# Performance work log

Hardware: AMD Instinct MI355X
Metric: run time of the kernel (lower is better)

Reference implementation:

```python
import jax, jax.numpy as jnp
import numpy as np

EPS = 1e-6
H, HD = 16, 64

def layernorm(x):
    m = jnp.mean(x, -1, keepdims=True)
    v = jnp.mean((x - m) ** 2, -1, keepdims=True)
    return (x - m) * jax.lax.rsqrt(v + EPS)

def rmsnorm(x, w):
    return x * jax.lax.rsqrt(jnp.mean(x * x, -1, keepdims=True) + EPS) * w

def apply_rope(x, rope_emb):
    # x: [B,S,H,D], rope_emb: [S,1,1,D] with cos||sin halves
    half = rope_emb.shape[-1] // 2
    cos = jnp.transpose(rope_emb[..., :half], (1, 0, 2, 3))  # [1,S,1,half]
    sin = jnp.transpose(rope_emb[..., half:], (1, 0, 2, 3))
    x1, x2 = x[..., :half], x[..., half:]
    rotated = jnp.concatenate([-x2, x1], -1)
    return x * jnp.concatenate([cos, cos], -1) + rotated * jnp.concatenate([sin, sin], -1)

def attention(xq, ctx, wq, wk, wv, wo, qn, kn, rope_emb):
    B, S, _ = xq.shape
    M = ctx.shape[1]
    q = (xq @ wq.T).reshape(B, S, H, HD)
    k = (ctx @ wk.T).reshape(B, M, H, HD)
    v = (ctx @ wv.T).reshape(B, M, H, HD)
    q = rmsnorm(q, qn)
    k = rmsnorm(k, kn)
    if rope_emb is not None:  # self-attn only
        q = apply_rope(q, rope_emb)
        k = apply_rope(k, rope_emb)
    # explicit bf16 cast before SDPA, as in torch_attention_op
    qb, kb, vb = (t.astype(jnp.bfloat16) for t in (q, k, v))
    scale = 1.0 / np.sqrt(HD).astype(np.float32)
    scores = jnp.einsum('bqhd,bkhd->bhqk', qb, kb) * scale
    probs = jax.nn.softmax(scores.astype(jnp.float32), -1).astype(jnp.bfloat16)
    out = jnp.einsum('bhqk,bkhd->bqhd', probs, vb)  # [B,S,H,HD]
    out = out.reshape(B, S, H * HD).astype(jnp.float32)
    return out @ wo.T

def modulation(emb, w):
    y = jax.nn.silu(emb) @ w.T  # [B, 3D]
    shift, scale, gate = jnp.split(y, 3, axis=-1)
    return shift[:, None], scale[:, None], gate[:, None]  # [B,1,D]

def setup_inputs() -> dict:
    key = jax.random.key(0)
    B, S, D, M, DF = 1, 4096, 1024, 512, 4096
    ks = jax.random.split(key, 20)
    std_d = 1.0 / np.sqrt(D)
    inp = {
        'x': jax.random.normal(ks[0], (B, S, D), jnp.float32),
        'emb': jax.random.normal(ks[1], (B, D), jnp.float32),
        'crossattn_emb': jax.random.normal(ks[2], (B, M, D), jnp.float32),
        'sa_wq': jax.random.normal(ks[3], (D, D), jnp.float32) * std_d,
        'sa_wk': jax.random.normal(ks[4], (D, D), jnp.float32) * std_d,
        'sa_wv': jax.random.normal(ks[5], (D, D), jnp.float32) * std_d,
        'sa_wo': jax.random.normal(ks[6], (D, D), jnp.float32) * std_d,
        'sa_qn': jnp.ones((HD,), jnp.float32),
        'sa_kn': jnp.ones((HD,), jnp.float32),
        'ca_wq': jax.random.normal(ks[7], (D, D), jnp.float32) * std_d,
        'ca_wk': jax.random.normal(ks[8], (D, D), jnp.float32) * std_d,
        'ca_wv': jax.random.normal(ks[9], (D, D), jnp.float32) * std_d,
        'ca_wo': jax.random.normal(ks[10], (D, D), jnp.float32) * std_d,
        'ca_qn': jnp.ones((HD,), jnp.float32),
        'ca_kn': jnp.ones((HD,), jnp.float32),
        'mlp_w1': jax.random.normal(ks[11], (DF, D), jnp.float32) * std_d,
        'mlp_w2': jax.random.normal(ks[12], (D, DF), jnp.float32) * (1.0 / np.sqrt(DF)),
        'mod_sa_w': jax.random.normal(ks[13], (3 * D, D), jnp.float32) * 0.02,
        'mod_ca_w': jax.random.normal(ks[14], (3 * D, D), jnp.float32) * 0.02,
        'mod_mlp_w': jax.random.normal(ks[15], (3 * D, D), jnp.float32) * 0.02,
    }
    # RoPE table [S,1,1,HD]: first half cos, second half sin
    pos = jnp.arange(S, dtype=jnp.float32)
    inv_freq = 1.0 / (10000.0 ** (jnp.arange(0, HD // 2, dtype=jnp.float32) / (HD // 2)))
    ang = pos[:, None] * inv_freq[None, :]  # [S, HD/2]
    inp['rope_emb'] = jnp.concatenate([jnp.cos(ang), jnp.sin(ang)], -1)[:, None, None, :]
    return inp

def reference(x, emb, crossattn_emb, rope_emb, sa_wq, sa_wk, sa_wv, sa_wo, sa_qn, sa_kn,
              ca_wq, ca_wk, ca_wv, ca_wo, ca_qn, ca_kn, mlp_w1, mlp_w2,
              mod_sa_w, mod_ca_w, mod_mlp_w):
    # self-attn with adaln modulation
    sh, sc, g = modulation(emb, mod_sa_w)
    h = layernorm(x) * (1.0 + sc) + sh
    x = x + g * attention(h, h, sa_wq, sa_wk, sa_wv, sa_wo, sa_qn, sa_kn, rope_emb)
    # cross-attn
    sh, sc, g = modulation(emb, mod_ca_w)
    h = layernorm(x) * (1.0 + sc) + sh
    x = x + g * attention(h, crossattn_emb, ca_wq, ca_wk, ca_wv, ca_wo, ca_qn, ca_kn, None)
    # mlp
    sh, sc, g = modulation(emb, mod_mlp_w)
    h = layernorm(x) * (1.0 + sc) + sh
    x = x + g * (jax.nn.gelu(h @ mlp_w1.T, approximate=False) @ mlp_w2.T)
    return x
```

## Files before the change

### kernel.cpp

```cpp
#include <hip/hip_runtime.h>
#include <hip/hip_bf16.h>

typedef __attribute__((ext_vector_type(8))) __bf16 bf16x8;
typedef __attribute__((ext_vector_type(4))) float f32x4;
typedef __attribute__((ext_vector_type(4))) unsigned short us4;

__device__ __forceinline__ unsigned short f2bf(float f){
  union { float f; unsigned int u; } a; a.f = f;
  unsigned int r = 0x7fffu + ((a.u >> 16) & 1u);
  return (unsigned short)((a.u + r) >> 16);
}

__device__ __forceinline__ unsigned int cvt_pk_bf16(float lo, float hi){
  unsigned int d;
  asm("v_cvt_pk_bf16_f32 %0, %1, %2" : "=v"(d) : "v"(lo), "v"(hi));
  return d;
}

__device__ __forceinline__ float exp2_hw(float x){
  float d;
  asm("v_exp_f32 %0, %1" : "=v"(d) : "v"(x));
  return d;
}

__device__ __forceinline__ void gload_lds16(const unsigned short* g, void* l){
  __builtin_amdgcn_global_load_lds(
      (const __attribute__((address_space(1))) void*)g,
      (__attribute__((address_space(3))) void*)l, 16, 0, 0);
}

struct CastJobs {
  const float* src[11];
  unsigned short* dst[11];
  int blkStart[12];
};

__global__ __launch_bounds__(256) void cast_all_kernel(CastJobs jobs){
  int bid = blockIdx.x;
  int j = 0;
  #pragma unroll
  for (int i = 0; i < 11; i++) j += (bid >= jobs.blkStart[i + 1]) ? 1 : 0;
  int i4 = (bid - jobs.blkStart[j]) * 256 + threadIdx.x;
  float4 v = ((const float4*)jobs.src[j])[i4];
  us4 o; o.x = f2bf(v.x); o.y = f2bf(v.y); o.z = f2bf(v.z); o.w = f2bf(v.w);
  ((us4*)jobs.dst[j])[i4] = o;
}

__global__ __launch_bounds__(256) void modulation_kernel(const float* __restrict__ emb,
    const float* __restrict__ w0, const float* __restrict__ w1, const float* __restrict__ w2,
    float* __restrict__ out){
  int gw = blockIdx.x * 4 + (threadIdx.x >> 6);
  int lane = threadIdx.x & 63;
  int mat = gw / 3072, row = gw % 3072;
  const float* w = (mat == 0) ? w0 : (mat == 1 ? w1 : w2);
  float acc = 0.f;
  for (int i = lane; i < 1024; i += 64){
    float e = emb[i];
    float s = e / (1.f + expf(-e));
    acc += s * w[row * 1024 + i];
  }
  #pragma unroll
  for (int m = 32; m >= 1; m >>= 1) acc += __shfl_xor(acc, m, 64);
  if (lane == 0) out[mat * 3072 + row] = acc;
}

__global__ __launch_bounds__(256) void ln_mod_kernel(const float* __restrict__ x,
    const float* __restrict__ mod, unsigned short* __restrict__ h){
  int row = blockIdx.x, t = threadIdx.x;
  const float* xr = x + (size_t)row * 1024;
  float4 v = ((const float4*)xr)[t];
  float s = v.x + v.y + v.z + v.w;
  #pragma unroll
  for (int m = 32; m >= 1; m >>= 1) s += __shfl_xor(s, m, 64);
  __shared__ float red[4], red2[4];
  int wid = t >> 6, lane = t & 63;
  if (lane == 0) red[wid] = s;
  __syncthreads();
  float mean = (red[0] + red[1] + red[2] + red[3]) * (1.f / 1024.f);
  float dx = v.x - mean, dy = v.y - mean, dz = v.z - mean, dw = v.w - mean;
  float s2 = dx*dx + dy*dy + dz*dz + dw*dw;
  #pragma unroll
  for (int m = 32; m >= 1; m >>= 1) s2 += __shfl_xor(s2, m, 64);
  if (lane == 0) red2[wid] = s2;
  __syncthreads();
  float var = (red2[0] + red2[1] + red2[2] + red2[3]) * (1.f / 1024.f);
  float rs = rsqrtf(var + 1e-6f);
  int c = t * 4;
  us4 o;
  o.x = f2bf(dx * rs * (1.f + mod[1024 + c    ]) + mod[c    ]);
  o.y = f2bf(dy * rs * (1.f + mod[1024 + c + 1]) + mod[c + 1]);
  o.z = f2bf(dz * rs * (1.f + mod[1024 + c + 2]) + mod[c + 2]);
  o.w = f2bf(dw * rs * (1.f + mod[1024 + c + 3]) + mod[c + 3]);
  ((us4*)(h + (size_t)row * 1024))[t] = o;
}

template<int ROPE>
__global__ __launch_bounds__(256) void qk_post2_kernel(
    const float* __restrict__ qin, const float* __restrict__ qnw,
    const float* __restrict__ kin, const float* __restrict__ knw,
    const float* __restrict__ rope,
    unsigned short* __restrict__ qout, unsigned short* __restrict__ kout,
    int Sq, int Sk, int qblocks){
  int bid = blockIdx.x;
  const float* in; const float* nw; unsigned short* out; int S;
  if (bid < qblocks){ in = qin; nw = qnw; out = qout; S = Sq; }
  else { in = kin; nw = knw; out = kout; S = Sk; bid -= qblocks; }
  int gw = bid * 4 + (threadIdx.x >> 6);
  int lane = threadIdx.x & 63;
  int s = gw >> 4, h = gw & 15;
  float v = in[(size_t)s * 1024 + h * 64 + lane];
  float ss = v * v;
  #pragma unroll
  for (int m = 32; m >= 1; m >>= 1) ss += __shfl_xor(ss, m, 64);
  float val = v * rsqrtf(ss * (1.f / 64.f) + 1e-6f) * nw[lane];
  if (ROPE){
    float partner = __shfl_xor(val, 32, 64);
    float cs = rope[s * 64 + (lane & 31)];
    float sn = rope[s * 64 + 32 + (lane & 31)];
    val = (lane < 32) ? (val * cs - partner * sn) : (val * cs + partner * sn);
  }
  out[((size_t)h * S + s) * 64 + lane] = f2bf(val);
}

__global__ __launch_bounds__(256) void vt_kernel(const float* __restrict__ Vf,
    unsigned short* __restrict__ Vt, int S){
  int stile = blockIdx.x, h = blockIdx.y;
  __shared__ unsigned short tile[64 * 66];
  int t = threadIdx.x;
  #pragma unroll
  for (int i = 0; i < 16; i++){
    int e = i * 256 + t;
    int srow = e >> 6, d = e & 63;
    tile[d * 66 + srow] = f2bf(Vf[(size_t)(stile * 64 + srow) * 1024 + h * 64 + d]);
  }
  __syncthreads();
  #pragma unroll
  for (int i = 0; i < 16; i++){
    int e = i * 256 + t;
    int d = e >> 6, scol = e & 63;
    Vt[((size_t)h * 64 + d) * S + stile * 64 + scol] = tile[d * 66 + scol];
  }
}

template<int EPI>
__global__ __launch_bounds__(256) void gemm_bt_kernel(
    const unsigned short* __restrict__ A, const unsigned short* __restrict__ W,
    int M, int N, int K,
    float* __restrict__ outF, unsigned short* __restrict__ outB,
    const float* __restrict__ resid, const float* __restrict__ gate){
  __shared__ short As[128 * 64];
  __shared__ short Bs[128 * 64];
  const int t = threadIdx.x, wid = t >> 6, lane = t & 63;
  const int r = lane & 15, g = lane >> 4;
  const int brow = blockIdx.y * 128, bcol = blockIdx.x * 128;
  const int wr = wid >> 1, wc = wid & 1;
  f32x4 acc[4][4] = {};
  const int nkt = K >> 6;
  for (int kt = 0; kt < nkt; ++kt){
    const int k0 = kt << 6;
    #pragma unroll
    for (int i = 0; i < 4; i++){
      int chunk = wid * 4 + i;
      int rowi = chunk * 8 + (lane >> 3);
      int lce = ((lane & 7) * 8) ^ ((rowi & 7) << 3);
      gload_lds16(A + (size_t)(brow + rowi) * K + k0 + lce, (void*)(As + chunk * 512));
      gload_lds16(W + (size_t)(bcol + rowi) * K + k0 + lce, (void*)(Bs + chunk * 512));
    }
    __syncthreads();
    #pragma unroll
    for (int kk = 0; kk < 2; kk++){
      bf16x8 af[4], bfr[4];
      #pragma unroll
      for (int m = 0; m < 4; m++){
        int ar = wr * 64 + m * 16 + r;
        af[m] = *(const bf16x8*)(As + ar * 64 + ((kk * 32 + g * 8) ^ ((ar & 7) << 3)));
      }
      #pragma unroll
      for (int n = 0; n < 4; n++){
        int br = wc * 64 + n * 16 + r;
        bfr[n] = *(const bf16x8*)(Bs + br * 64 + ((kk * 32 + g * 8) ^ ((br & 7) << 3)));
      }
      #pragma unroll
      for (int m = 0; m < 4; m++)
        #pragma unroll
        for (int n = 0; n < 4; n++)
          acc[m][n] = __builtin_amdgcn_mfma_f32_16x16x32_bf16(af[m], bfr[n], acc[m][n], 0, 0, 0);
    }
    __syncthreads();
  }
  #pragma unroll
  for (int m = 0; m < 4; m++){
    #pragma unroll
    for (int n = 0; n < 4; n++){
      int col = bcol + wc * 64 + n * 16 + r;
      #pragma unroll
      for (int j = 0; j < 4; j++){
        int rowj = brow + wr * 64 + m * 16 + g * 4 + j;
        float v = acc[m][n][j];
        if (EPI == 0){
          outF[(size_t)rowj * N + col] = v;
        } else if (EPI == 2){
          float gl = 0.5f * v * (1.f + erff(v * 0.70710678118654752f));
          outB[(size_t)rowj * N + col] = f2bf(gl);
        } else if (EPI == 4){
          outF[(size_t)(col >> 10) * 4194304 + (size_t)rowj * 1024 + (col & 1023)] = v;
        } else {
          outF[(size_t)rowj * N + col] = resid[(size_t)rowj * N + col] + gate[col] * v;
        }
      }
    }
  }
}

template<int EPI>
__global__ __launch_bounds__(256) void gemm_bt64_kernel(
    const unsigned short* __restrict__ A, const unsigned short* __restrict__ W,
    int M, int N, int K,
    float* __restrict__ outF, unsigned short* __restrict__ outB,
    const float* __restrict__ resid, const float* __restrict__ gate){
  __shared__ short As[64 * 64];
  __shared__ short Bs[128 * 64];
  const int t = threadIdx.x, wid = t >> 6, lane = t & 63;
  const int r = lane & 15, g = lane >> 4;
  const int brow = blockIdx.y * 64, bcol = blockIdx.x * 128;
  f32x4 acc[4][2] = {};
  const int nkt = K >> 6;
  const int sr = lane >> 3;
  const int lce = ((lane & 7) * 8) ^ ((sr & 7) << 3);
  for (int kt = 0; kt < nkt; ++kt){
    const int k0 = kt << 6;
    #pragma unroll
    for (int i = 0; i < 2; i++){
      int chunk = wid * 2 + i;
      gload_lds16(A + (size_t)(brow + chunk * 8 + sr) * K + k0 + lce, (void*)(As + chunk * 512));
    }
    #pragma unroll
    for (int i = 0; i < 4; i++){
      int chunk = wid * 4 + i;
      gload_lds16(W + (size_t)(bcol + chunk * 8 + sr) * K + k0 + lce, (void*)(Bs + chunk * 512));
    }
    __syncthreads();
    #pragma unroll
    for (int kk = 0; kk < 2; kk++){
      bf16x8 af[4], bfr[2];
      #pragma unroll
      for (int m = 0; m < 4; m++){
        int ar = m * 16 + r;
        af[m] = *(const bf16x8*)(As + ar * 64 + ((kk * 32 + g * 8) ^ ((ar & 7) << 3)));
      }
      #pragma unroll
      for (int n = 0; n < 2; n++){
        int br = wid * 32 + n * 16 + r;
        bfr[n] = *(const bf16x8*)(Bs + br * 64 + ((kk * 32 + g * 8) ^ ((br & 7) << 3)));
      }
      #pragma unroll
      for (int m = 0; m < 4; m++)
        #pragma unroll
        for (int n = 0; n < 2; n++)
          acc[m][n] = __builtin_amdgcn_mfma_f32_16x16x32_bf16(af[m], bfr[n], acc[m][n], 0, 0, 0);
    }
    __syncthreads();
  }
  #pragma unroll
  for (int m = 0; m < 4; m++){
    #pragma unroll
    for (int n = 0; n < 2; n++){
      int col = bcol + wid * 32 + n * 16 + r;
      #pragma unroll
      for (int j = 0; j < 4; j++){
        int rowj = brow + m * 16 + g * 4 + j;
        float v = acc[m][n][j];
        if (EPI == 0){
          outF[(size_t)rowj * N + col] = v;
        } else if (EPI == 4){
          outF[(size_t)(col >> 10) * 4194304 + (size_t)rowj * 1024 + (col & 1023)] = v;
        } else {
          outF[(size_t)rowj * N + col] = resid[(size_t)rowj * N + col] + gate[col] * v;
        }
      }
    }
  }
}

__global__ __launch_bounds__(256) void gemm_bt64_sk_kernel(
    const unsigned short* __restrict__ A, const unsigned short* __restrict__ W,
    int M, int N, int K, float* __restrict__ outP){
  __shared__ short As[64 * 64];
  __shared__ short Bs[128 * 64];
  const int t = threadIdx.x, wid = t >> 6, lane = t & 63;
  const int r = lane & 15, g = lane >> 4;
  const int brow = blockIdx.y * 64, bcol = blockIdx.x * 128;
  const int zk = blockIdx.z;
  const int koff = zk * (K >> 1);
  float* out = outP + (size_t)zk * 4194304;
  f32x4 acc[4][2] = {};
  const int nkt = K >> 7;
  const int sr = lane >> 3;
  const int lce = ((lane & 7) * 8) ^ ((sr & 7) << 3);
  for (int kt = 0; kt < nkt; ++kt){
    const int k0 = koff + (kt << 6);
    #pragma unroll
    for (int i = 0; i < 2; i++){
      int chunk = wid * 2 + i;
      gload_lds16(A + (size_t)(brow + chunk * 8 + sr) * K + k0 + lce, (void*)(As + chunk * 512));
    }
    #pragma unroll
    for (int i = 0; i < 4; i++){
      int chunk = wid * 4 + i;
      gload_lds16(W + (size_t)(bcol + chunk * 8 + sr) * K + k0 + lce, (void*)(Bs + chunk * 512));
    }
    __syncthreads();
    #pragma unroll
    for (int kk = 0; kk < 2; kk++){
      bf16x8 af[4], bfr[2];
      #pragma unroll
      for (int m = 0; m < 4; m++){
        int ar = m * 16 + r;
        af[m] = *(const bf16x8*)(As + ar * 64 + ((kk * 32 + g * 8) ^ ((ar & 7) << 3)));
      }
      #pragma unroll
      for (int n = 0; n < 2; n++){
        int br = wid * 32 + n * 16 + r;
        bfr[n] = *(const bf16x8*)(Bs + br * 64 + ((kk * 32 + g * 8) ^ ((br & 7) << 3)));
      }
      #pragma unroll
      for (int m = 0; m < 4; m++)
        #pragma unroll
        for (int n = 0; n < 2; n++)
          acc[m][n] = __builtin_amdgcn_mfma_f32_16x16x32_bf16(af[m], bfr[n], acc[m][n], 0, 0, 0);
    }
    __syncthreads();
  }
  #pragma unroll
  for (int m = 0; m < 4; m++){
    #pragma unroll
    for (int n = 0; n < 2; n++){
      int col = bcol + wid * 32 + n * 16 + r;
      #pragma unroll
      for (int j = 0; j < 4; j++){
        int rowj = brow + m * 16 + g * 4 + j;
        out[(size_t)rowj * N + col] = acc[m][n][j];
      }
    }
  }
}

__global__ __launch_bounds__(256) void reduce_gg_kernel(const float* __restrict__ p0,
    const float* __restrict__ p1, const float* __restrict__ gate, float* __restrict__ xio){
  int i4 = blockIdx.x * 256 + threadIdx.x;
  float4 a = ((const float4*)p0)[i4];
  float4 b = ((const float4*)p1)[i4];
  float4 rr = ((const float4*)xio)[i4];
  int col = (i4 * 4) & 1023;
  float4 gv = *(const float4*)&gate[col];
  float4 o;
  o.x = rr.x + gv.x * (a.x + b.x);
  o.y = rr.y + gv.y * (a.y + b.y);
  o.z = rr.z + gv.z * (a.z + b.z);
  o.w = rr.w + gv.w * (a.w + b.w);
  ((float4*)xio)[i4] = o;
}

__global__ __launch_bounds__(256) void attn_kernel(
    const unsigned short* __restrict__ Qb, const unsigned short* __restrict__ Kb,
    const unsigned short* __restrict__ Vtg, unsigned short* __restrict__ Out,
    int Sq, int Skv){
  __shared__ short Ks[3][4096];
  __shared__ short Vs[3][4096];
  __shared__ unsigned short Ps[4][2048];
  const int t = threadIdx.x, wid = t >> 6, lane = t & 63;
  const int r = lane & 15, g = lane >> 4;
  const int bid = blockIdx.x;
  const int slot = bid >> 3;
  const int h = (bid & 7) * 2 + (slot >> 5);
  const int qblk = slot & 31;
  const int qbase = qblk * 128 + wid * 32;
  const float SC = 0.18033688f;
  const float MS = 12.0f;

  const int srow0 = wid * 16 + (lane >> 3);
  const int scol  = ((lane & 7) * 8) ^ (((lane >> 3) & 7) << 3);
  const unsigned short* kSrc0 = Kb + ((size_t)h * Skv + srow0) * 64 + scol;
  const unsigned short* kSrc1 = kSrc0 + 8 * 64;
  const unsigned short* vSrc0 = Vtg + ((size_t)h * 64 + srow0) * Skv + scol;
  const unsigned short* vSrc1 = vSrc0 + (size_t)8 * Skv;

  bf16x8 qf[2][2];
  #pragma unroll
  for (int qt = 0; qt < 2; qt++){
    const unsigned short* qp = Qb + ((size_t)h * Sq + qbase + qt * 16 + r) * 64 + g * 8;
    qf[qt][0] = *(const bf16x8*)qp;
    qf[qt][1] = *(const bf16x8*)(qp + 32);
  }
  f32x4 o[2][4] = {};
  f32x4 lacc[2] = {};

  const int nkv = Skv >> 6;

  gload_lds16(kSrc0, (void*)&Ks[0][(wid * 2 + 0) * 512]);
  gload_lds16(kSrc1, (void*)&Ks[0][(wid * 2 + 1) * 512]);
  gload_lds16(vSrc0, (void*)&Vs[0][(wid * 2 + 0) * 512]);
  gload_lds16(vSrc1, (void*)&Vs[0][(wid * 2 + 1) * 512]);
  gload_lds16(kSrc0 + 4096, (void*)&Ks[1][(wid * 2 + 0) * 512]);
  gload_lds16(kSrc1 + 4096, (void*)&Ks[1][(wid * 2 + 1) * 512]);
  gload_lds16(vSrc0 + 64, (void*)&Vs[1][(wid * 2 + 0) * 512]);
  gload_lds16(vSrc1 + 64, (void*)&Vs[1][(wid * 2 + 1) * 512]);
  asm volatile("s_waitcnt vmcnt(4)" ::: "memory");
  __builtin_amdgcn_s_barrier();

  int cur = 0, stg = 2;
  for (int it = 0; it < nkv; ++it){
    if (it + 2 < nkv){
      size_t ko = (size_t)(it + 2) << 12;
      size_t vo = (size_t)(it + 2) << 6;
      gload_lds16(kSrc0 + ko, (void*)&Ks[stg][(wid * 2 + 0) * 512]);
      gload_lds16(kSrc1 + ko, (void*)&Ks[stg][(wid * 2 + 1) * 512]);
      gload_lds16(vSrc0 + vo, (void*)&Vs[stg][(wid * 2 + 0) * 512]);
      gload_lds16(vSrc1 + vo, (void*)&Vs[stg][(wid * 2 + 1) * 512]);
    }
    const short* kb = &Ks[cur][0];
    const short* vb = &Vs[cur][0];

    f32x4 pT[2][4];
    __builtin_amdgcn_s_setprio(1);
    #pragma unroll
    for (int kt = 0; kt < 4; kt++){
      int kr = kt * 16 + r;
      bf16x8 k0 = *(const bf16x8*)(kb + kr * 64 + ((g * 8) ^ ((kr & 7) << 3)));
      bf16x8 k1 = *(const bf16x8*)(kb + kr * 64 + ((32 + g * 8) ^ ((kr & 7) << 3)));
      #pragma unroll
      for (int qt = 0; qt < 2; qt++){
        f32x4 a = {};
        a = __builtin_amdgcn_mfma_f32_16x16x32_bf16(k0, qf[qt][0], a, 0, 0, 0);
        a = __builtin_amdgcn_mfma_f32_16x16x32_bf16(k1, qf[qt][1], a, 0, 0, 0);
        pT[qt][kt] = a;
      }
    }
    __builtin_amdgcn_s_setprio(0);

    #pragma unroll
    for (int qt = 0; qt < 2; qt++){
      unsigned short* pw = &Ps[wid][(qt * 16 + r) * 64];
      int rx = (r & 7) << 3;
      #pragma unroll
      for (int kt = 0; kt < 4; kt++){
        f32x4 pe;
        #pragma unroll
        for (int e = 0; e < 4; e++) pe[e] = exp2_hw(fmaf(pT[qt][kt][e], SC, -MS));
        lacc[qt] += pe;
        unsigned int w0 = cvt_pk_bf16(pe[0], pe[1]);
        unsigned int w1 = cvt_pk_bf16(pe[2], pe[3]);
        *(uint2*)(pw + ((kt * 16 + g * 4) ^ rx)) = make_uint2(w0, w1);
      }
    }

    __builtin_amdgcn_s_setprio(1);
    {
      bf16x8 pf[2][2];
      int rx = (r & 7) << 3;
      #pragma unroll
      for (int qt = 0; qt < 2; qt++){
        const unsigned short* pw = &Ps[wid][(qt * 16 + r) * 64];
        pf[qt][0] = *(const bf16x8*)(pw + ((g * 8) ^ rx));
        pf[qt][1] = *(const bf16x8*)(pw + ((32 + g * 8) ^ rx));
      }
      #pragma unroll
      for (int dj = 0; dj < 4; dj++){
        int vrow = dj * 16 + r;
        bf16x8 v0 = *(const bf16x8*)(vb + vrow * 64 + ((g * 8) ^ ((vrow & 7) << 3)));
        bf16x8 v1 = *(const bf16x8*)(vb + vrow * 64 + ((32 + g * 8) ^ ((vrow & 7) << 3)));
        #pragma unroll
        for (int qt = 0; qt < 2; qt++){
          o[qt][dj] = __builtin_amdgcn_mfma_f32_16x16x32_bf16(pf[qt][0], v0, o[qt][dj], 0, 0, 0);
          o[qt][dj] = __builtin_amdgcn_mfma_f32_16x16x32_bf16(pf[qt][1], v1, o[qt][dj], 0, 0, 0);
        }
      }
    }
    __builtin_amdgcn_s_setprio(0);

    if (it + 1 < nkv){
      if (it + 2 < nkv) asm volatile("s_waitcnt vmcnt(4)" ::: "memory");
      else              asm volatile("s_waitcnt vmcnt(0)" ::: "memory");
      __builtin_amdgcn_s_barrier();
    }
    cur = (cur == 2) ? 0 : cur + 1;
    stg = (stg == 2) ? 0 : stg + 1;
  }

  #pragma unroll
  for (int qt = 0; qt < 2; qt++){
    float s = (lacc[qt][0] + lacc[qt][1]) + (lacc[qt][2] + lacc[qt][3]);
    s += __shfl_xor(s, 16, 64);
    s += __shfl_xor(s, 32, 64);
    float inv = 1.f / s;
    int sb = lane & 48;
    #pragma unroll
    for (int j = 0; j < 4; j++){
      float aj = __shfl(inv, sb + g * 4 + j, 64);
      int qrow = qbase + qt * 16 + g * 4 + j;
      #pragma unroll
      for (int dj = 0; dj < 4; dj++)
        Out[(size_t)qrow * 1024 + h * 64 + dj * 16 + r] = f2bf(o[qt][dj][j] * aj);
    }
  }
}

extern "C" void kernel_launch(void* const* d_in, const int* in_sizes, int n_in,
                              void* d_out, int out_size, void* d_ws, size_t ws_size,
                              hipStream_t stream){
  (void)n_in; (void)out_size;
  const float* x   = (const float*)d_in[0];
  const float* emb = (const float*)d_in[1];
  const float* ctx = (const float*)d_in[2];
  int wb = 3, ri = 20;
  if (in_sizes[3] == 4096 * 64) { ri = 3; wb = 4; }
  const float* rope  = (const float*)d_in[ri];
  const float* sa_wq = (const float*)d_in[wb + 0];
  const float* sa_wk = (const float*)d_in[wb + 1];
  const float* sa_wv = (const float*)d_in[wb + 2];
  const float* sa_wo = (const float*)d_in[wb + 3];
  const float* sa_qn = (const float*)d_in[wb + 4];
  const float* sa_kn = (const float*)d_in[wb + 5];
  const float* ca_wq = (const float*)d_in[wb + 6];
  const float* ca_wk = (const float*)d_in[wb + 7];
  const float* ca_wv = (const float*)d_in[wb + 8];
  const float* ca_wo = (const float*)d_in[wb + 9];
  const float* ca_qn = (const float*)d_in[wb + 10];
  const float* ca_kn = (const float*)d_in[wb + 11];
  const float* w1    = (const float*)d_in[wb + 12];
  const float* w2    = (const float*)d_in[wb + 13];
  const float* msa   = (const float*)d_in[wb + 14];
  const float* mca   = (const float*)d_in[wb + 15];
  const float* mmlp  = (const float*)d_in[wb + 16];

  char* ws = (char*)d_ws;
  const size_t MB = 1u << 20;
  if (ws_size < 114 * MB) return;
  unsigned short* wq_sa = (unsigned short*)(ws + 0 * MB);
  unsigned short* wk_sa = (unsigned short*)(ws + 2 * MB);
  unsigned short* wv_sa = (unsigned short*)(ws + 4 * MB);
  unsigned short* wo_sa = (unsigned short*)(ws + 6 * MB);
  unsigned short* wq_ca = (unsigned short*)(ws + 8 * MB);
  unsigned short* wk_ca = (unsigned short*)(ws + 10 * MB);
  unsigned short* wv_ca = (unsigned short*)(ws + 12 * MB);
  unsigned short* wo_ca = (unsigned short*)(ws + 14 * MB);
  unsigned short* w1bf  = (unsigned short*)(ws + 16 * MB);
  unsigned short* w2bf  = (unsigned short*)(ws + 24 * MB);
  unsigned short* ctxbf = (unsigned short*)(ws + 32 * MB);
  float*          modv  = (float*)(ws + 33 * MB);
  unsigned short* hbf   = (unsigned short*)(ws + 34 * MB);
  unsigned short* qbf   = (unsigned short*)(ws + 42 * MB);
  unsigned short* kbf   = (unsigned short*)(ws + 50 * MB);
  unsigned short* aobf  = (unsigned short*)(ws + 58 * MB);
  float*          qf32  = (float*)(ws + 66 * MB);
  float*          kf32  = (float*)(ws + 82 * MB);
  float*          vf32  = (float*)(ws + 98 * MB);
  unsigned short* vtb   = (unsigned short*)(ws + 82 * MB);
  unsigned short* midbf = (unsigned short*)(ws + 66 * MB);
  float*          mp0   = (float*)(ws + 34 * MB);
  float*          mp1   = (float*)(ws + 50 * MB);
  float* xcur = (float*)d_out;

  CastJobs cj;
  const float* srcs[11] = {sa_wq, sa_wk, sa_wv, sa_wo, ca_wq, ca_wk, ca_wv, ca_wo, w1, w2, ctx};
  unsigned short* dsts[11] = {wq_sa, wk_sa, wv_sa, wo_sa, wq_ca, wk_ca, wv_ca, wo_ca, w1bf, w2bf, ctxbf};
  int n4s[11] = {262144, 262144, 262144, 262144, 262144, 262144, 262144, 262144, 1048576, 1048576, 131072};
  int cum = 0;
  for (int i = 0; i < 11; i++){
    cj.src[i] = srcs[i]; cj.dst[i] = dsts[i];
    cj.blkStart[i] = cum; cum += n4s[i] / 256;
  }
  cj.blkStart[11] = cum;
  cast_all_kernel<<<cum, 256, 0, stream>>>(cj);
  modulation_kernel<<<2304, 256, 0, stream>>>(emb, msa, mca, mmlp, modv);

  ln_mod_kernel<<<4096, 256, 0, stream>>>(x, modv + 0 * 3072, hbf);
  gemm_bt_kernel<4><<<dim3(24, 32), 256, 0, stream>>>(hbf, wq_sa, 4096, 3072, 1024, qf32, nullptr, nullptr, nullptr);
  qk_post2_kernel<1><<<32768, 256, 0, stream>>>(qf32, sa_qn, kf32, sa_kn, rope, qbf, kbf, 4096, 4096, 16384);
  vt_kernel<<<dim3(64, 16), 256, 0, stream>>>(vf32, vtb, 4096);
  attn_kernel<<<512, 256, 0, stream>>>(qbf, kbf, vtb, aobf, 4096, 4096);
  gemm_bt64_kernel<3><<<dim3(8, 64), 256, 0, stream>>>(aobf, wo_sa, 4096, 1024, 1024, xcur, nullptr, x, modv + 0 * 3072 + 2048);

  ln_mod_kernel<<<4096, 256, 0, stream>>>(xcur, modv + 1 * 3072, hbf);
  gemm_bt64_kernel<0><<<dim3(8, 64), 256, 0, stream>>>(hbf, wq_ca, 4096, 1024, 1024, qf32, nullptr, nullptr, nullptr);
  gemm_bt64_kernel<4><<<dim3(16, 8), 256, 0, stream>>>(ctxbf, wk_ca, 512, 2048, 1024, kf32, nullptr, nullptr, nullptr);
  qk_post2_kernel<0><<<18432, 256, 0, stream>>>(qf32, ca_qn, kf32, ca_kn, nullptr, qbf, kbf, 4096, 512, 16384);
  vt_kernel<<<dim3(8, 16), 256, 0, stream>>>(vf32, vtb, 512);
  attn_kernel<<<512, 256, 0, stream>>>(qbf, kbf, vtb, aobf, 4096, 512);
  gemm_bt64_kernel<3><<<dim3(8, 64), 256, 0, stream>>>(aobf, wo_ca, 4096, 1024, 1024, xcur, nullptr, xcur, modv + 1 * 3072 + 2048);

  ln_mod_kernel<<<4096, 256, 0, stream>>>(xcur, modv + 2 * 3072, hbf);
  gemm_bt_kernel<2><<<dim3(32, 32), 256, 0, stream>>>(hbf, w1bf, 4096, 4096, 1024, nullptr, midbf, nullptr, nullptr);
  gemm_bt64_sk_kernel<<<dim3(8, 64, 2), 256, 0, stream>>>(midbf, w2bf, 4096, 1024, 4096, mp0);
  reduce_gg_kernel<<<4096, 256, 0, stream>>>(mp0, mp1, modv + 2 * 3072 + 2048, xcur);
}
```

Before: 441.2 us.

## Fuse V transpose into QKV GEMM epilogue and use tanh-form GELU

Adds a GEMM epilogue mode that writes K (and Q) columns as fp32 but stores V columns directly as transposed bf16. This removes the separate V transpose kernels and the fp32 V buffer round trip for both self- and cross-attention. It also replaces the erf-based GELU in the MLP epilogue with a tanh approximation built from hardware exp and reciprocal. The transposed stores are strided and poorly coalesced, and the GELU approximation deviates from the exact erf form the reference requires.

```diff
diff --git a/kernel.cpp b/kernel.cpp
--- a/kernel.cpp
+++ b/kernel.cpp
@@ -20,6 +20,12 @@
 __device__ __forceinline__ float exp2_hw(float x){
   float d;
   asm("v_exp_f32 %0, %1" : "=v"(d) : "v"(x));
+  return d;
+}
+
+__device__ __forceinline__ float rcp_hw(float x){
+  float d;
+  asm("v_rcp_f32 %0, %1" : "=v"(d) : "v"(x));
   return d;
 }
 
@@ -122,32 +128,13 @@
   out[((size_t)h * S + s) * 64 + lane] = f2bf(val);
 }
 
-__global__ __launch_bounds__(256) void vt_kernel(const float* __restrict__ Vf,
-    unsigned short* __restrict__ Vt, int S){
-  int stile = blockIdx.x, h = blockIdx.y;
-  __shared__ unsigned short tile[64 * 66];
-  int t = threadIdx.x;
-  #pragma unroll
-  for (int i = 0; i < 16; i++){
-    int e = i * 256 + t;
-    int srow = e >> 6, d = e & 63;
-    tile[d * 66 + srow] = f2bf(Vf[(size_t)(stile * 64 + srow) * 1024 + h * 64 + d]);
-  }
-  __syncthreads();
-  #pragma unroll
-  for (int i = 0; i < 16; i++){
-    int e = i * 256 + t;
-    int d = e >> 6, scol = e & 63;
-    Vt[((size_t)h * 64 + d) * S + stile * 64 + scol] = tile[d * 66 + scol];
-  }
-}
-
 template<int EPI>
 __global__ __launch_bounds__(256) void gemm_bt_kernel(
     const unsigned short* __restrict__ A, const unsigned short* __restrict__ W,
     int M, int N, int K,
     float* __restrict__ outF, unsigned short* __restrict__ outB,
-    const float* __restrict__ resid, const float* __restrict__ gate){
+    const float* __restrict__ resid, const float* __restrict__ gate,
+    int vstart, int Sv){
   __shared__ short As[128 * 64];
   __shared__ short Bs[128 * 64];
   const int t = threadIdx.x, wid = t >> 6, lane = t & 63;
@@ -200,10 +187,19 @@
         if (EPI == 0){
           outF[(size_t)rowj * N + col] = v;
         } else if (EPI == 2){
-          float gl = 0.5f * v * (1.f + erff(v * 0.70710678118654752f));
+          float u = v * fmaf(v * v, 0.044715f, 1.0f);
+          float e = exp2_hw(u * 2.3022077f);
+          float gl = v * (1.f - rcp_hw(e + 1.f));
           outB[(size_t)rowj * N + col] = f2bf(gl);
         } else if (EPI == 4){
           outF[(size_t)(col >> 10) * 4194304 + (size_t)rowj * 1024 + (col & 1023)] = v;
+        } else if (EPI == 5){
+          if (col < vstart){
+            outF[(size_t)(col >> 10) * 4194304 + (size_t)rowj * 1024 + (col & 1023)] = v;
+          } else {
+            int vc = col - vstart;
+            outB[(size_t)vc * Sv + rowj] = f2bf(v);
+          }
         } else {
           outF[(size_t)rowj * N + col] = resid[(size_t)rowj * N + col] + gate[col] * v;
         }
@@ -217,7 +213,8 @@
     const unsigned short* __restrict__ A, const unsigned short* __restrict__ W,
     int M, int N, int K,
     float* __restrict__ outF, unsigned short* __restrict__ outB,
-    const float* __restrict__ resid, const float* __restrict__ gate){
+    const float* __restrict__ resid, const float* __restrict__ gate,
+    int vstart, int Sv){
   __shared__ short As[64 * 64];
   __shared__ short Bs[128 * 64];
   const int t = threadIdx.x, wid = t >> 6, lane = t & 63;
@@ -274,6 +271,13 @@
           outF[(size_t)rowj * N + col] = v;
         } else if (EPI == 4){
           outF[(size_t)(col >> 10) * 4194304 + (size_t)rowj * 1024 + (col & 1023)] = v;
+        } else if (EPI == 5){
+          if (col < vstart){
+            outF[(size_t)(col >> 10) * 4194304 + (size_t)rowj * 1024 + (col & 1023)] = v;
+          } else {
+            int vc = col - vstart;
+            outB[(size_t)vc * Sv + rowj] = f2bf(v);
+          }
         } else {
           outF[(size_t)rowj * N + col] = resid[(size_t)rowj * N + col] + gate[col] * v;
         }
@@ -553,9 +557,8 @@
   unsigned short* kbf   = (unsigned short*)(ws + 50 * MB);
   unsigned short* aobf  = (unsigned short*)(ws + 58 * MB);
   float*          qf32  = (float*)(ws + 66 * MB);
-  float*          kf32  = (float*)(ws + 82 * MB);
-  float*          vf32  = (float*)(ws + 98 * MB);
-  unsigned short* vtb   = (unsigned short*)(ws + 82 * MB);
+  float*          kca32 = (float*)(ws + 82 * MB);
+  unsigned short* vtb   = (unsigned short*)(ws + 98 * MB);
   unsigned short* midbf = (unsigned short*)(ws + 66 * MB);
   float*          mp0   = (float*)(ws + 34 * MB);
   float*          mp1   = (float*)(ws + 50 * MB);
@@ -575,22 +578,20 @@
   modulation_kernel<<<2304, 256, 0, stream>>>(emb, msa, mca, mmlp, modv);
 
   ln_mod_kernel<<<4096, 256, 0, stream>>>(x, modv + 0 * 3072, hbf);
-  gemm_bt_kernel<4><<<dim3(24, 32), 256, 0, stream>>>(hbf, wq_sa, 4096, 3072, 1024, qf32, nullptr, nullptr, nullptr);
-  qk_post2_kernel<1><<<32768, 256, 0, stream>>>(qf32, sa_qn, kf32, sa_kn, rope, qbf, kbf, 4096, 4096, 16384);
-  vt_kernel<<<dim3(64, 16), 256, 0, stream>>>(vf32, vtb, 4096);
+  gemm_bt_kernel<5><<<dim3(24, 32), 256, 0, stream>>>(hbf, wq_sa, 4096, 3072, 1024, qf32, vtb, nullptr, nullptr, 2048, 4096);
+  qk_post2_kernel<1><<<32768, 256, 0, stream>>>(qf32, sa_qn, qf32 + 4194304, sa_kn, rope, qbf, kbf, 4096, 4096, 16384);
   attn_kernel<<<512, 256, 0, stream>>>(qbf, kbf, vtb, aobf, 4096, 4096);
-  gemm_bt64_kernel<3><<<dim3(8, 64), 256, 0, stream>>>(aobf, wo_sa, 4096, 1024, 1024, xcur, nullptr, x, modv + 0 * 3072 + 2048);
+  gemm_bt64_kernel<3><<<dim3(8, 64), 256, 0, stream>>>(aobf, wo_sa, 4096, 1024, 1024, xcur, nullptr, x, modv + 0 * 3072 + 2048, 0, 0);
 
   ln_mod_kernel<<<4096, 256, 0, stream>>>(xcur, modv + 1 * 3072, hbf);
-  gemm_bt64_kernel<0><<<dim3(8, 64), 256, 0, stream>>>(hbf, wq_ca, 4096, 1024, 1024, qf32, nullptr, nullptr, nullptr);
-  gemm_bt64_kernel<4><<<dim3(16, 8), 256, 0, stream>>>(ctxbf, wk_ca, 512, 2048, 1024, kf32, nullptr, nullptr, nullptr);
-  qk_post2_kernel<0><<<18432, 256, 0, stream>>>(qf32, ca_qn, kf32, ca_kn, nullptr, qbf, kbf, 4096, 512, 16384);
-  vt_kernel<<<dim3(8, 16), 256, 0, stream>>>(vf32, vtb, 512);
+  gemm_bt64_kernel<0><<<dim3(8, 64), 256, 0, stream>>>(hbf, wq_ca, 4096, 1024, 1024, qf32, nullptr, nullptr, nullptr, 0, 0);
+  gemm_bt64_kernel<5><<<dim3(16, 8), 256, 0, stream>>>(ctxbf, wk_ca, 512, 2048, 1024, kca32, vtb, nullptr, nullptr, 1024, 512);
+  qk_post2_kernel<0><<<18432, 256, 0, stream>>>(qf32, ca_qn, kca32, ca_kn, nullptr, qbf, kbf, 4096, 512, 16384);
   attn_kernel<<<512, 256, 0, stream>>>(qbf, kbf, vtb, aobf, 4096, 512);
-  gemm_bt64_kernel<3><<<dim3(8, 64), 256, 0, stream>>>(aobf, wo_ca, 4096, 1024, 1024, xcur, nullptr, xcur, modv + 1 * 3072 + 2048);
+  gemm_bt64_kernel<3><<<dim3(8, 64), 256, 0, stream>>>(aobf, wo_ca, 4096, 1024, 1024, xcur, nullptr, xcur, modv + 1 * 3072 + 2048, 0, 0);
 
   ln_mod_kernel<<<4096, 256, 0, stream>>>(xcur, modv + 2 * 3072, hbf);
-  gemm_bt_kernel<2><<<dim3(32, 32), 256, 0, stream>>>(hbf, w1bf, 4096, 4096, 1024, nullptr, midbf, nullptr, nullptr);
+  gemm_bt_kernel<2><<<dim3(32, 32), 256, 0, stream>>>(hbf, w1bf, 4096, 4096, 1024, nullptr, midbf, nullptr, nullptr, 0, 0);
   gemm_bt64_sk_kernel<<<dim3(8, 64, 2), 256, 0, stream>>>(midbf, w2bf, 4096, 1024, 4096, mp0);
   reduce_gg_kernel<<<4096, 256, 0, stream>>>(mp0, mp1, modv + 2 * 3072 + 2048, xcur);
 }
```

Measured after the change: 440.2 us. Within noise of the previous version (-0.2%).
